# Optimization experiments

Hardware: AMD Instinct MI355X
Metric: run time of the kernel (lower is better)

The kernel has to match this reference:

```python
import jax, jax.numpy as jnp
import numpy as np

S, B, H, N, D = 1024, 4, 1024, 16, 64  # seq, batch, d_model, heads, head_dim
P = 2 * S  # relative position length (klen + qlen, no memory)


def rel_shift(x, klen):
    # x: [q, p, b, n] -> shift so position j aligns relatively, keep klen cols
    q, p, b, n = x.shape
    x = jnp.reshape(x, (p, q, b, n))[1:]
    x = jnp.reshape(x, (q, p - 1, b, n))[:, :klen]
    return x


def setup_inputs():
    key = jax.random.key(0)
    ks = jax.random.split(key, 12)
    f32 = jnp.float32
    attention_input = jax.random.normal(ks[0], (S, B, H), f32)
    pos_emb = jax.random.normal(ks[1], (P, B, H), f32)
    seg_embed = jax.random.normal(ks[2], (2, N, D), f32) * 0.02
    # segment matrix: one-hot of whether tokens i,j are in different segments
    seg_ids = jax.random.randint(ks[3], (S, B), 0, 2)
    diff = (seg_ids[:, None, :] != seg_ids[None, :, :]).astype(jnp.int32)
    seg_mat = jax.nn.one_hot(diff, 2, dtype=f32)  # [S,S,B,2]
    r_w_bias = jax.random.normal(ks[4], (N, D), f32) * 0.02
    r_r_bias = jax.random.normal(ks[5], (N, D), f32) * 0.02
    r_s_bias = jax.random.normal(ks[6], (N, D), f32) * 0.02
    # causal mask: 1 where attention is disallowed (j > i)
    causal = jnp.triu(jnp.ones((S, S), f32), k=1)
    attn_mask = jnp.broadcast_to(causal[:, :, None, None], (S, S, B, 1))
    w = lambda k: jax.random.normal(k, (H, N, D), f32) * 0.02
    return {
        'attention_input': attention_input, 'pos_emb': pos_emb,
        'seg_embed': seg_embed, 'seg_mat': seg_mat,
        'r_w_bias': r_w_bias, 'r_r_bias': r_r_bias, 'r_s_bias': r_s_bias,
        'attn_mask': attn_mask,
        'Wq': w(ks[7]), 'Wk': w(ks[8]), 'Wv': w(ks[9]),
        'Wr': w(ks[10]), 'Wo': w(ks[11]),
    }


def reference(attention_input, pos_emb, seg_embed, seg_mat, r_w_bias,
              r_r_bias, r_s_bias, attn_mask, Wq, Wk, Wv, Wr, Wo):
    scale = 1.0 / (D ** 0.5)
    q = jnp.einsum('ibh,hnd->ibnd', attention_input, Wq)
    k = jnp.einsum('ibh,hnd->ibnd', attention_input, Wk)
    v = jnp.einsum('ibh,hnd->ibnd', attention_input, Wv)
    kr = jnp.einsum('ibh,hnd->ibnd', pos_emb, Wr)  # [P,B,N,D]
    # content-based score
    ac = jnp.einsum('ibnd,jbnd->ijbn', q + r_w_bias, k)
    # position-based score with relative shift
    bd = jnp.einsum('ibnd,jbnd->ijbn', q + r_r_bias, kr)
    bd = rel_shift(bd, ac.shape[1])
    # segment-based score
    ef = jnp.einsum('ibnd,snd->ibns', q + r_s_bias, seg_embed)
    ef = jnp.einsum('ijbs,ibns->ijbn', seg_mat, ef)
    attn_score = (ac + bd + ef) * scale - 1e30 * attn_mask
    attn_prob = jax.nn.softmax(attn_score, axis=1)
    attn_vec = jnp.einsum('ijbn,jbnd->ibnd', attn_prob, v)
    attn_out = jnp.einsum('ibnd,hnd->ibh', attn_vec, Wo)
    return attn_out
```

## Files before the change

kernel.cpp:

```cpp
#include <hip/hip_runtime.h>
#include <hip/hip_bf16.h>
#include <stdint.h>


typedef short short8 __attribute__((ext_vector_type(8)));
typedef __bf16 bf16x8 __attribute__((ext_vector_type(8)));
typedef float f32x4 __attribute__((ext_vector_type(4)));
typedef unsigned short u16;
typedef unsigned long long u64;

#define LOG2E 1.4426950408889634f

__device__ __forceinline__ u16 f2bf(float f) {
  union { float f; unsigned u; } v; v.f = f;
  unsigned u = v.u;
  u += 0x7fffu + ((u >> 16) & 1u);
  return (u16)(u >> 16);
}
__device__ __forceinline__ float bf2f(u16 h) {
  union { unsigned u; float f; } v; v.u = ((unsigned)h) << 16;
  return v.f;
}

__device__ __forceinline__ f32x4 MFMA(short8 a, short8 b, f32x4 c) {
  union { short8 s; bf16x8 v; } ua, ub;
  ua.s = a; ub.s = b;
  return __builtin_amdgcn_mfma_f32_16x16x32_bf16(ua.v, ub.v, c, 0, 0, 0);
}

__device__ __forceinline__ void gload16(const void* g, void* l) {
  __builtin_amdgcn_global_load_lds(
      (const __attribute__((address_space(1))) unsigned int*)g,
      (__attribute__((address_space(3))) unsigned int*)l, 16, 0, 0);
}


__global__ void k_cvt3(const float* __restrict__ pos, const float* __restrict__ X,
                       const float* __restrict__ Wo, u16* __restrict__ Pb,
                       u16* __restrict__ Xb, u16* __restrict__ Wob) {
  int bid = blockIdx.x;
  const float* in; u16* out; int n, base;
  if (bid < 4101)      { in = pos; out = Pb;  n = 4198400; base = bid; }
  else if (bid < 8197) { in = X;   out = Xb;  n = 4194304; base = bid - 4101; }
  else                 { in = Wo;  out = Wob; n = 1048576; base = bid - 8197; }
  int i = (base * 256 + threadIdx.x) * 4;
  if (i >= n) return;
  float4 f = *reinterpret_cast<const float4*>(in + i);
  ushort4 o;
  o.x = f2bf(f.x); o.y = f2bf(f.y); o.z = f2bf(f.z); o.w = f2bf(f.w);
  *reinterpret_cast<ushort4*>(out + i) = o;
}

__global__ void k_transpose(const float* __restrict__ Wq, const float* __restrict__ Wk,
                            const float* __restrict__ Wv, const float* __restrict__ Wr,
                            u16* __restrict__ WT3, u16* __restrict__ WrT) {
  __shared__ float tile[32][33];
  int which = blockIdx.z;
  const float* src = (which == 0) ? Wq : (which == 1) ? Wk : (which == 2) ? Wv : Wr;
  u16* dst = (which < 3) ? (WT3 + (size_t)which * 1048576) : WrT;
  int c0 = blockIdx.x * 32, h0 = blockIdx.y * 32;
  int tx = threadIdx.x, ty = threadIdx.y;
  for (int r = 0; r < 32; r += 8)
    tile[ty + r][tx] = src[(size_t)(h0 + ty + r) * 1024 + c0 + tx];
  __syncthreads();
  for (int r = 0; r < 32; r += 8)
    dst[(size_t)(c0 + ty + r) * 1024 + h0 + tx] = f2bf(tile[tx][ty + r]);
}

__global__ void k_vt(const u16* __restrict__ V, u16* __restrict__ VT) {
  __shared__ u16 t[64][68];
  int i0 = blockIdx.x * 64;
  int bn = blockIdx.y;
  int tx = threadIdx.x;
  int ty = threadIdx.y;
#pragma unroll
  for (int q = 0; q < 16; q++) {
    int il = ty * 16 + q;
    t[il][tx] = V[(size_t)((bn << 10) + i0 + il) * 64 + tx];
  }
  __syncthreads();
#pragma unroll
  for (int q = 0; q < 16; q++) {
    int d = ty * 16 + q;
    VT[(((size_t)((bn << 6) | d)) << 10) + i0 + tx] = t[tx][d];
  }
}

__global__ void k_dpackw(const float* __restrict__ seg, u64* __restrict__ dpw) {
  int W = blockIdx.x * 4 + (threadIdx.x >> 6);
  int lane = threadIdx.x & 63;
  int jt = W & 15, i = W >> 4;
  const float4* p = reinterpret_cast<const float4*>(
      seg + ((size_t)((i << 10) + (jt << 6) + lane)) * 8);
  float4 a = p[0], bq = p[1];
  u64 m0 = __ballot(a.y != 0.f);
  u64 m1 = __ballot(a.w != 0.f);
  u64 m2 = __ballot(bq.y != 0.f);
  u64 m3 = __ballot(bq.w != 0.f);
  if (lane == 0) {
    int o = (i << 4) + jt;
    dpw[o] = m0;
    dpw[16384 + o] = m1;
    dpw[32768 + o] = m2;
    dpw[49152 + o] = m3;
  }
}

__global__ void k_ef(const u16* __restrict__ Q, const float* __restrict__ rsb,
                     const float* __restrict__ segE, float* __restrict__ ef) {
  int idx = blockIdx.x * blockDim.x + threadIdx.x;
  if (idx >= 65536) return;
  int n = (idx >> 10) & 15;
  float s0 = 0.f, s1 = 0.f;
  const short8* qrow = reinterpret_cast<const short8*>(Q + ((size_t)idx) * 64);
#pragma unroll
  for (int c = 0; c < 8; c++) {
    short8 v = qrow[c];
#pragma unroll
    for (int e = 0; e < 8; e++) {
      int d = c * 8 + e;
      float qv = bf2f((u16)v[e]) + rsb[n * 64 + d];
      s0 += qv * segE[n * 64 + d];
      s1 += qv * segE[1024 + n * 64 + d];
    }
  }
  ef[idx] = s0 * 0.125f;
  ef[65536 + idx] = s1 * 0.125f;
}


template <int MODE>
__device__ __forceinline__ int srcA(int row, int kk) {
  if (MODE == 0) return row * 1024 + kk;
  if (MODE == 1) return ((1024 - (row >> 2)) * 4 + (row & 3)) * 1024 + kk;
  int i = row >> 2, b = row & 3, n = kk >> 6, d = kk & 63;
  return (((b << 4) | n) * 1024 + i) * 64 + d;
}

template <int MODE>
__global__ __launch_bounds__(256, 2) void k_gemm(const u16* __restrict__ A,
                                                 const u16* __restrict__ L,
                                                 void* __restrict__ out0,
                                                 u16* __restrict__ outK,
                                                 u16* __restrict__ outV) {
  __shared__ u16 At[128 * 32];
  __shared__ u16 Lt[128 * 32];
  int m0 = blockIdx.x * 128, n0 = blockIdx.y * 128;
  int tid = threadIdx.x;
  int w = tid >> 6, lane = tid & 63;
  int lr = lane & 15, lg = lane >> 4;
  int wr = w >> 1, wc = w & 1;
  f32x4 acc[4][4] = {};

  for (int k0 = 0; k0 < 1024; k0 += 32) {
    for (int cc = 0; cc < 2; cc++) {
      int slot = cc * 256 + w * 64 + lane;
      int row = slot >> 2, ch = slot & 3;
      int sch = ch ^ ((row >> 1) & 3);
      gload16(A + srcA<MODE>(m0 + row, k0 + sch * 8), &At[(cc * 256 + w * 64) * 8]);
      gload16(L + (size_t)(n0 + row) * 1024 + k0 + sch * 8, &Lt[(cc * 256 + w * 64) * 8]);
    }
    __syncthreads();
    short8 af[4], bfr[4];
    for (int mt = 0; mt < 4; mt++) {
      int rr = wr * 64 + mt * 16 + lr;
      af[mt] = *reinterpret_cast<const short8*>(&At[rr * 32 + ((lg ^ ((rr >> 1) & 3)) * 8)]);
    }
    for (int ct = 0; ct < 4; ct++) {
      int rr = wc * 64 + ct * 16 + lr;
      bfr[ct] = *reinterpret_cast<const short8*>(&Lt[rr * 32 + ((lg ^ ((rr >> 1) & 3)) * 8)]);
    }
    for (int mt = 0; mt < 4; mt++)
      for (int ct = 0; ct < 4; ct++)
        acc[mt][ct] = MFMA(af[mt], bfr[ct], acc[mt][ct]);
    __syncthreads();
  }

  for (int mt = 0; mt < 4; mt++)
    for (int ct = 0; ct < 4; ct++)
      for (int r = 0; r < 4; r++) {
        int row = m0 + wr * 64 + mt * 16 + lg * 4 + r;
        int col = n0 + wc * 64 + ct * 16 + lr;
        float v = acc[mt][ct][r];
        if (MODE == 0) {
          int i = row >> 2, b = row & 3;
          int which = col >> 10, nd = col & 1023, n = nd >> 6, d = nd & 63;
          u16 hv = f2bf(v);
          int bn = (b << 4) | n;
          if (which == 0)       ((u16*)out0)[(size_t)(bn * 1024 + i) * 64 + d] = hv;
          else if (which == 1)  outK[(size_t)(bn * 1024 + i) * 64 + d] = hv;
          else                  outV[(size_t)(bn * 1024 + i) * 64 + d] = hv;
        } else if (MODE == 1) {
          int dist = row >> 2, b = row & 3, n = col >> 6, d = col & 63;
          ((u16*)out0)[(size_t)((((b << 4) | n) * 1024 + dist)) * 64 + d] = f2bf(v);
        } else {
          ((float*)out0)[(size_t)row * 1024 + col] = v;
        }
      }
}

__global__ __launch_bounds__(256, 2) void k_attn3(
    const u16* __restrict__ Q, const u16* __restrict__ K, const u16* __restrict__ VT,
    const u16* __restrict__ R, const float* __restrict__ ef,
    const u64* __restrict__ dpw, const float* __restrict__ rwb,
    const float* __restrict__ rrb, float* __restrict__ lsb, u16* __restrict__ pO) {
  __shared__ u16 sK[2][64][64];
  __shared__ u16 sV[2][64][64];
  __shared__ u16 sR[2][128][64];
  __shared__ u16 p_lds[4][16][64];
  int f = blockIdx.x + 40 * blockIdx.y;
  int wg = (f & 7) * 320 + (f >> 3);
  int bn = wg / 40;
  int cid = 39 - (wg - bn * 40);
  int b = bn >> 4, n = bn & 15;
  int g = (cid < 4) ? 0 : (cid < 12) ? 1 : (cid < 24) ? 2 : 3;
  int off = cid - 2 * g * (g + 1);
  int qt = 4 * g + off / (g + 1);
  int jc = off % (g + 1);
  int ntiles = (jc < g) ? 4 : (qt + 1 - 4 * g);
  int jt0 = jc * 4;
  int tid = threadIdx.x;
  int w = tid >> 6, lane = tid & 63;
  int lr = lane & 15, lg = lane >> 4;
  int qbase = qt * 64 + w * 16;
  int sub = lane >> 3, ch = lane & 7;
  int cs = (ch ^ sub) * 8;
  int r8 = lr & 7;

  auto stage = [&](int bi, int j0) {
    int rbase = qt * 64 - j0 - 63;
#pragma unroll
    for (int q = 0; q < 2; q++) {
      int row = w * 16 + q * 8 + sub;
      gload16(K + (size_t)((bn << 10) + j0 + row) * 64 + cs, &sK[bi][w * 16 + q * 8][0]);
      gload16(VT + (((size_t)((bn << 6) + row)) << 10) + j0 + cs, &sV[bi][w * 16 + q * 8][0]);
    }
#pragma unroll
    for (int q = 0; q < 4; q++) {
      int pr = w * 32 + q * 8 + sub;
      int ridx = rbase + pr;
      ridx = ridx < 0 ? 0 : (ridx > 1023 ? 1023 : ridx);
      gload16(R + (size_t)((bn << 10) + ridx) * 64 + cs, &sR[bi][w * 32 + q * 8][0]);
    }
  };

  stage(0, jt0 * 64);

  const u64* dwbase = dpw + ((size_t)((b << 10) + qbase + lg * 4) << 4);
  u64 dwc[4], dwn[4] = {0, 0, 0, 0};
#pragma unroll
  for (int r = 0; r < 4; r++) dwc[r] = dwbase[(r << 4) + jt0];

  short8 qw[2], qr[2];
  for (int ks = 0; ks < 2; ks++) {
    short8 qv = *reinterpret_cast<const short8*>(
        &Q[(size_t)((bn << 10) + qbase + lr) * 64 + ks * 32 + lg * 8]);
    short8 aa, bb;
    for (int e = 0; e < 8; e++) {
      int d = ks * 32 + lg * 8 + e;
      float fq = bf2f((u16)qv[e]);
      aa[e] = (short)f2bf((fq + rwb[n * 64 + d]) * 0.125f);
      bb[e] = (short)f2bf((fq + rrb[n * 64 + d]) * 0.125f);
    }
    qw[ks] = aa;
    qr[ks] = bb;
  }
  short8 ones;
#pragma unroll
  for (int e = 0; e < 8; e++) ones[e] = (short)0x3F80;
  float e0[4], de[4];
  for (int r = 0; r < 4; r++) {
    int qi = qbase + lg * 4 + r;
    e0[r] = ef[(bn << 10) + qi];
    de[r] = ef[65536 + (bn << 10) + qi] - e0[r];
  }
  float lsum[4] = {0.f, 0.f, 0.f, 0.f};
  f32x4 Oacc[4] = {};

  for (int t = 0; t < ntiles; t++) {
    int jt = jt0 + t;
    int j0 = jt * 64;
    int bi = t & 1;
    asm volatile("s_waitcnt vmcnt(0)" ::: "memory");
    __syncthreads();
    if (t + 1 < ntiles) {
      stage(bi ^ 1, j0 + 64);
#pragma unroll
      for (int r = 0; r < 4; r++) dwn[r] = dwbase[(r << 4) + jt + 1];
    }

    f32x4 sacc[4] = {};
    f32x4 tacc[5] = {};
    __builtin_amdgcn_s_setprio(1);
#pragma unroll
    for (int ks = 0; ks < 2; ks++) {
#pragma unroll
      for (int ct = 0; ct < 4; ct++) {
        short8 kb = *reinterpret_cast<const short8*>(
            &sK[bi][ct * 16 + lr][((ks * 4 + lg) ^ r8) * 8]);
        sacc[ct] = MFMA(qw[ks], kb, sacc[ct]);
      }
#pragma unroll
      for (int ct = 0; ct < 5; ct++) {
        short8 rb = *reinterpret_cast<const short8*>(
            &sR[bi][w * 16 + ct * 16 + lr][((ks * 4 + lg) ^ r8) * 8]);
        tacc[ct] = MFMA(qr[ks], rb, tacc[ct]);
      }
    }
    __builtin_amdgcn_s_setprio(0);

    bool diag = (jt == qt);
#pragma unroll
    for (int r = 0; r < 4; r++) {
      int ii = lg * 4 + r;
      int C0 = 63 + ii - lr;
      int sl = (lg << 4) | (C0 & 15);
      bool hi = (C0 >> 4) == 3;
      float tp0 = __shfl(tacc[0][r], sl);
      float tp1 = __shfl(tacc[1][r], sl);
      float tp2 = __shfl(tacc[2][r], sl);
      float tp3 = __shfl(tacc[3][r], sl);
      float tp4 = __shfl(tacc[4][r], sl);
#pragma unroll
      for (int ct = 0; ct < 4; ct++) {
        float bd;
        if (ct == 0)      bd = hi ? tp3 : tp4;
        else if (ct == 1) bd = hi ? tp2 : tp3;
        else if (ct == 2) bd = hi ? tp1 : tp2;
        else              bd = hi ? tp0 : tp1;
        float s = sacc[ct][r] + bd + e0[r];
        int jj = ct * 16 + lr;
        if ((dwc[r] >> jj) & 1) s += de[r];
        if (diag && jj > w * 16 + ii) s = -1.0e30f;
        sacc[ct][r] = exp2f(s * LOG2E);
      }
    }
#pragma unroll
    for (int ct = 0; ct < 4; ct++)
#pragma unroll
      for (int r = 0; r < 4; r++) {
        int ii = lg * 4 + r, jj = ct * 16 + lr;
        p_lds[w][ii][jj ^ ((ii & 7) << 3)] = f2bf(sacc[ct][r]);
      }
    f32x4 so = {};
    __builtin_amdgcn_s_setprio(1);
#pragma unroll
    for (int ks = 0; ks < 2; ks++) {
      int chunk = ks * 4 + lg;
      short8 afr = *reinterpret_cast<const short8*>(&p_lds[w][lr][(chunk ^ (lr & 7)) * 8]);
      so = MFMA(afr, ones, so);
#pragma unroll
      for (int dt = 0; dt < 4; dt++) {
        short8 vb = *reinterpret_cast<const short8*>(
            &sV[bi][dt * 16 + lr][((ks * 4 + lg) ^ r8) * 8]);
        Oacc[dt] = MFMA(afr, vb, Oacc[dt]);
      }
    }
    __builtin_amdgcn_s_setprio(0);
#pragma unroll
    for (int r = 0; r < 4; r++) lsum[r] += so[r];
#pragma unroll
    for (int r = 0; r < 4; r++) dwc[r] = dwn[r];
  }

  int pid = bn * 40 + cid;
  if (lr == 0)
#pragma unroll
    for (int r = 0; r < 4; r++) {
      int row = w * 16 + lg * 4 + r;
      lsb[(size_t)pid * 64 + row] = lsum[r];
    }
#pragma unroll
  for (int dt = 0; dt < 4; dt++)
#pragma unroll
    for (int r = 0; r < 4; r++) {
      int row = w * 16 + lg * 4 + r;
      pO[(size_t)pid * 4096 + row * 64 + dt * 16 + lr] = f2bf(Oacc[dt][r]);
    }
}

__global__ void k_comb(const float* __restrict__ lsb, const u16* __restrict__ pO,
                       u16* __restrict__ AV) {
  __shared__ float sinv[64];
  int qt = blockIdx.x, bn = blockIdx.y;
  int g = qt >> 2, nc = g + 1;
  int cbase = 2 * g * (g + 1) + (qt - 4 * g) * (g + 1);
  int pid0 = bn * 40 + cbase;
  int t = threadIdx.x;
  if (t < 64) {
    float L = 0.f;
    for (int c2 = 0; c2 < 4; c2++)
      if (c2 < nc) L += lsb[(size_t)(pid0 + c2) * 64 + t];
    sinv[t] = 1.0f / L;
  }
  __syncthreads();
  int dg = t & 7, rowg = t >> 3;
  for (int half = 0; half < 2; half++) {
    int ii = half * 32 + rowg;
    float o[8] = {0, 0, 0, 0, 0, 0, 0, 0};
    for (int c2 = 0; c2 < 4; c2++) {
      if (c2 >= nc) break;
      short8 pv = *reinterpret_cast<const short8*>(
          &pO[(size_t)(pid0 + c2) * 4096 + ii * 64 + dg * 8]);
      for (int e2 = 0; e2 < 8; e2++) o[e2] += bf2f((u16)pv[e2]);
    }
    float s = sinv[ii];
    short8 ov;
    for (int e2 = 0; e2 < 8; e2++) ov[e2] = (short)f2bf(o[e2] * s);
    *reinterpret_cast<short8*>(&AV[(size_t)((bn << 10) + qt * 64 + ii) * 64 + dg * 8]) = ov;
  }
}


extern "C" void kernel_launch(void* const* d_in, const int* in_sizes, int n_in,
                              void* d_out, int out_size, void* d_ws, size_t ws_size,
                              hipStream_t stream) {
  const float* X    = (const float*)d_in[0];
  const float* pos  = (const float*)d_in[1];
  const float* segE = (const float*)d_in[2];
  const float* segM = (const float*)d_in[3];
  const float* rwb  = (const float*)d_in[4];
  const float* rrb  = (const float*)d_in[5];
  const float* rsb  = (const float*)d_in[6];
  const float* Wq = (const float*)d_in[8];
  const float* Wk = (const float*)d_in[9];
  const float* Wv = (const float*)d_in[10];
  const float* Wr = (const float*)d_in[11];
  const float* Wo = (const float*)d_in[12];

  char* ws = (char*)d_ws;
  u16* Xb   = (u16*)(ws);
  u16* Pb   = (u16*)(ws + (8L << 20));
  u16* WT3  = (u16*)(ws + (24L << 20));
  u16* WrT  = (u16*)(ws + (30L << 20));
  u16* Wob  = (u16*)(ws + (32L << 20));
  u16* Qb   = (u16*)(ws + (34L << 20));
  u16* Kb   = (u16*)(ws + (42L << 20));
  u16* VTb  = (u16*)(ws + (50L << 20));
  u16* Rb   = (u16*)(ws + (58L << 20));
  float* efb = (float*)(ws + (66L << 20));
  u64* dpwb = (u64*)(ws + (66L << 20) + (512L << 10));
  float* lsbb = (float*)(ws + (67L << 20));
  u16* pOb  = (u16*)(ws + (69L << 20));
  u16* AVb  = Xb;
  u16* Vtmp = Pb;

  k_cvt3<<<9221, 256, 0, stream>>>(pos, X, Wo, Pb, Xb, Wob);
  k_transpose<<<dim3(32, 32, 4), dim3(32, 8), 0, stream>>>(Wq, Wk, Wv, Wr, WT3, WrT);
  k_gemm<1><<<dim3(32, 8), 256, 0, stream>>>(Pb, WrT, Rb, nullptr, nullptr);
  k_dpackw<<<4096, 256, 0, stream>>>(segM, dpwb);
  k_gemm<0><<<dim3(32, 24), 256, 0, stream>>>(Xb, WT3, Qb, Kb, Vtmp);
  k_vt<<<dim3(16, 64), dim3(64, 4), 0, stream>>>(Vtmp, VTb);
  k_ef<<<256, 256, 0, stream>>>(Qb, rsb, segE, efb);
  k_attn3<<<dim3(40, 64), 256, 0, stream>>>(Qb, Kb, VTb, Rb, efb, dpwb, rwb, rrb, lsbb, pOb);
  k_comb<<<dim3(16, 64), 256, 0, stream>>>(lsbb, pOb, AVb);
  k_gemm<2><<<dim3(32, 8), 256, 0, stream>>>(AVb, Wob, d_out, nullptr, nullptr);
}
```

Measured before the change: 177.9 us.

## Merge prep kernels, fuse QKV and R GEMMs, write single-chunk attention output directly

Merges the conversion, weight transpose and segment-bitmask kernels into one launch, and the V transpose plus ef kernels into another. Runs the QKV and positional-key GEMMs in one grid. Folds log2(e) into the Q scaling and ef so the exp2 needs no extra multiply. Attention blocks whose query tile has a single key chunk now normalize and write AV directly, so the combine kernel skips those tiles. This cuts launch count and tail idle time between small kernels, at the cost of branchy, heterogeneous blocks in the merged kernels.

```diff
diff --git a/kernel.cpp b/kernel.cpp
--- a/kernel.cpp
+++ b/kernel.cpp
@@ -34,118 +34,130 @@
       (__attribute__((address_space(3))) unsigned int*)l, 16, 0, 0);
 }
 
-
-__global__ void k_cvt3(const float* __restrict__ pos, const float* __restrict__ X,
-                       const float* __restrict__ Wo, u16* __restrict__ Pb,
-                       u16* __restrict__ Xb, u16* __restrict__ Wob) {
+__global__ void k_prep(const float* __restrict__ pos, const float* __restrict__ X,
+                       const float* __restrict__ Wo, const float* __restrict__ Wq,
+                       const float* __restrict__ Wk, const float* __restrict__ Wv,
+                       const float* __restrict__ Wr, const float* __restrict__ seg,
+                       u16* __restrict__ Pb, u16* __restrict__ Xb, u16* __restrict__ Wob,
+                       u16* __restrict__ WT3, u16* __restrict__ WrT, u64* __restrict__ dpw) {
   int bid = blockIdx.x;
-  const float* in; u16* out; int n, base;
-  if (bid < 4101)      { in = pos; out = Pb;  n = 4198400; base = bid; }
-  else if (bid < 8197) { in = X;   out = Xb;  n = 4194304; base = bid - 4101; }
-  else                 { in = Wo;  out = Wob; n = 1048576; base = bid - 8197; }
-  int i = (base * 256 + threadIdx.x) * 4;
-  if (i >= n) return;
-  float4 f = *reinterpret_cast<const float4*>(in + i);
-  ushort4 o;
-  o.x = f2bf(f.x); o.y = f2bf(f.y); o.z = f2bf(f.z); o.w = f2bf(f.w);
-  *reinterpret_cast<ushort4*>(out + i) = o;
-}
-
-__global__ void k_transpose(const float* __restrict__ Wq, const float* __restrict__ Wk,
-                            const float* __restrict__ Wv, const float* __restrict__ Wr,
-                            u16* __restrict__ WT3, u16* __restrict__ WrT) {
-  __shared__ float tile[32][33];
-  int which = blockIdx.z;
-  const float* src = (which == 0) ? Wq : (which == 1) ? Wk : (which == 2) ? Wv : Wr;
-  u16* dst = (which < 3) ? (WT3 + (size_t)which * 1048576) : WrT;
-  int c0 = blockIdx.x * 32, h0 = blockIdx.y * 32;
-  int tx = threadIdx.x, ty = threadIdx.y;
-  for (int r = 0; r < 32; r += 8)
-    tile[ty + r][tx] = src[(size_t)(h0 + ty + r) * 1024 + c0 + tx];
-  __syncthreads();
-  for (int r = 0; r < 32; r += 8)
-    dst[(size_t)(c0 + ty + r) * 1024 + h0 + tx] = f2bf(tile[tx][ty + r]);
-}
-
-__global__ void k_vt(const u16* __restrict__ V, u16* __restrict__ VT) {
-  __shared__ u16 t[64][68];
-  int i0 = blockIdx.x * 64;
-  int bn = blockIdx.y;
-  int tx = threadIdx.x;
-  int ty = threadIdx.y;
-#pragma unroll
-  for (int q = 0; q < 16; q++) {
-    int il = ty * 16 + q;
-    t[il][tx] = V[(size_t)((bn << 10) + i0 + il) * 64 + tx];
-  }
-  __syncthreads();
-#pragma unroll
-  for (int q = 0; q < 16; q++) {
-    int d = ty * 16 + q;
-    VT[(((size_t)((bn << 6) | d)) << 10) + i0 + tx] = t[tx][d];
-  }
-}
-
-__global__ void k_dpackw(const float* __restrict__ seg, u64* __restrict__ dpw) {
-  int W = blockIdx.x * 4 + (threadIdx.x >> 6);
-  int lane = threadIdx.x & 63;
-  int jt = W & 15, i = W >> 4;
-  const float4* p = reinterpret_cast<const float4*>(
-      seg + ((size_t)((i << 10) + (jt << 6) + lane)) * 8);
-  float4 a = p[0], bq = p[1];
-  u64 m0 = __ballot(a.y != 0.f);
-  u64 m1 = __ballot(a.w != 0.f);
-  u64 m2 = __ballot(bq.y != 0.f);
-  u64 m3 = __ballot(bq.w != 0.f);
-  if (lane == 0) {
-    int o = (i << 4) + jt;
-    dpw[o] = m0;
-    dpw[16384 + o] = m1;
-    dpw[32768 + o] = m2;
-    dpw[49152 + o] = m3;
-  }
-}
-
-__global__ void k_ef(const u16* __restrict__ Q, const float* __restrict__ rsb,
-                     const float* __restrict__ segE, float* __restrict__ ef) {
-  int idx = blockIdx.x * blockDim.x + threadIdx.x;
-  if (idx >= 65536) return;
-  int n = (idx >> 10) & 15;
-  float s0 = 0.f, s1 = 0.f;
-  const short8* qrow = reinterpret_cast<const short8*>(Q + ((size_t)idx) * 64);
-#pragma unroll
-  for (int c = 0; c < 8; c++) {
-    short8 v = qrow[c];
-#pragma unroll
-    for (int e = 0; e < 8; e++) {
-      int d = c * 8 + e;
-      float qv = bf2f((u16)v[e]) + rsb[n * 64 + d];
-      s0 += qv * segE[n * 64 + d];
-      s1 += qv * segE[1024 + n * 64 + d];
-    }
-  }
-  ef[idx] = s0 * 0.125f;
-  ef[65536 + idx] = s1 * 0.125f;
-}
-
-
-template <int MODE>
-__device__ __forceinline__ int srcA(int row, int kk) {
-  if (MODE == 0) return row * 1024 + kk;
-  if (MODE == 1) return ((1024 - (row >> 2)) * 4 + (row & 3)) * 1024 + kk;
+  int tid = threadIdx.x;
+  if (bid < 9221) {
+    const float* in; u16* out; int n, base;
+    if (bid < 4101)      { in = pos; out = Pb;  n = 4198400; base = bid; }
+    else if (bid < 8197) { in = X;   out = Xb;  n = 4194304; base = bid - 4101; }
+    else                 { in = Wo;  out = Wob; n = 1048576; base = bid - 8197; }
+    int i = (base * 256 + tid) * 4;
+    if (i >= n) return;
+    float4 f = *reinterpret_cast<const float4*>(in + i);
+    ushort4 o;
+    o.x = f2bf(f.x); o.y = f2bf(f.y); o.z = f2bf(f.z); o.w = f2bf(f.w);
+    *reinterpret_cast<ushort4*>(out + i) = o;
+  } else if (bid < 13317) {
+    __shared__ float tile[32][33];
+    int tb = bid - 9221;
+    int which = tb >> 10;
+    int by = (tb >> 5) & 31, bx = tb & 31;
+    const float* src = (which == 0) ? Wq : (which == 1) ? Wk : (which == 2) ? Wv : Wr;
+    u16* dst = (which < 3) ? (WT3 + (size_t)which * 1048576) : WrT;
+    int c0 = bx * 32, h0 = by * 32;
+    int tx = tid & 31, ty = tid >> 5;
+    for (int r = 0; r < 32; r += 8)
+      tile[ty + r][tx] = src[(size_t)(h0 + ty + r) * 1024 + c0 + tx];
+    __syncthreads();
+    for (int r = 0; r < 32; r += 8)
+      dst[(size_t)(c0 + ty + r) * 1024 + h0 + tx] = f2bf(tile[tx][ty + r]);
+  } else {
+    int W = (bid - 13317) * 4 + (tid >> 6);
+    int lane = tid & 63;
+    int jt = W & 15, i = W >> 4;
+    const float4* p = reinterpret_cast<const float4*>(
+        seg + ((size_t)((i << 10) + (jt << 6) + lane)) * 8);
+    float4 a = p[0], bq = p[1];
+    u64 m0 = __ballot(a.y != 0.f);
+    u64 m1 = __ballot(a.w != 0.f);
+    u64 m2 = __ballot(bq.y != 0.f);
+    u64 m3 = __ballot(bq.w != 0.f);
+    if (lane == 0) {
+      int o = (i << 4) + jt;
+      dpw[o] = m0;
+      dpw[16384 + o] = m1;
+      dpw[32768 + o] = m2;
+      dpw[49152 + o] = m3;
+    }
+  }
+}
+
+__global__ void k_mid(const u16* __restrict__ V, u16* __restrict__ VT,
+                      const u16* __restrict__ Q, const float* __restrict__ rsb,
+                      const float* __restrict__ segE, float* __restrict__ ef) {
+  int bid = blockIdx.x;
+  int tid = threadIdx.x;
+  if (bid < 1024) {
+    __shared__ u16 t[64][68];
+    int i0 = (bid & 15) * 64;
+    int bn = bid >> 4;
+    int tx = tid & 63, ty = tid >> 6;
+#pragma unroll
+    for (int q = 0; q < 16; q++) {
+      int il = ty * 16 + q;
+      t[il][tx] = V[(size_t)((bn << 10) + i0 + il) * 64 + tx];
+    }
+    __syncthreads();
+#pragma unroll
+    for (int q = 0; q < 16; q++) {
+      int d = ty * 16 + q;
+      VT[(((size_t)((bn << 6) | d)) << 10) + i0 + tx] = t[tx][d];
+    }
+  } else {
+    int idx = (bid - 1024) * 256 + tid;
+    int n = (idx >> 10) & 15;
+    float s0 = 0.f, s1 = 0.f;
+    const short8* qrow = reinterpret_cast<const short8*>(Q + ((size_t)idx) * 64);
+#pragma unroll
+    for (int c = 0; c < 8; c++) {
+      short8 v = qrow[c];
+#pragma unroll
+      for (int e = 0; e < 8; e++) {
+        int d = c * 8 + e;
+        float qv = bf2f((u16)v[e]) + rsb[n * 64 + d];
+        s0 += qv * segE[n * 64 + d];
+        s1 += qv * segE[1024 + n * 64 + d];
+      }
+    }
+    ef[idx] = s0 * (0.125f * LOG2E);
+    ef[65536 + idx] = s1 * (0.125f * LOG2E);
+  }
+}
+
+
+__device__ __forceinline__ int srcA_g(int mode, int row, int kk) {
+  if (mode == 0) return row * 1024 + kk;
+  if (mode == 1) return ((1024 - (row >> 2)) * 4 + (row & 3)) * 1024 + kk;
   int i = row >> 2, b = row & 3, n = kk >> 6, d = kk & 63;
   return (((b << 4) | n) * 1024 + i) * 64 + d;
 }
 
-template <int MODE>
-__global__ __launch_bounds__(256, 2) void k_gemm(const u16* __restrict__ A,
-                                                 const u16* __restrict__ L,
+template <int FUSED01>
+__global__ __launch_bounds__(256, 2) void k_gemm(const u16* __restrict__ A0,
+                                                 const u16* __restrict__ L0,
+                                                 const u16* __restrict__ A1,
+                                                 const u16* __restrict__ L1,
                                                  void* __restrict__ out0,
                                                  u16* __restrict__ outK,
-                                                 u16* __restrict__ outV) {
+                                                 u16* __restrict__ outV,
+                                                 u16* __restrict__ outR) {
   __shared__ u16 At[128 * 32];
   __shared__ u16 Lt[128 * 32];
-  int m0 = blockIdx.x * 128, n0 = blockIdx.y * 128;
+  int mode, n0;
+  const u16 *A, *L;
+  if (FUSED01) {
+    if (blockIdx.y < 24) { mode = 0; n0 = blockIdx.y * 128; A = A0; L = L0; }
+    else                 { mode = 1; n0 = (blockIdx.y - 24) * 128; A = A1; L = L1; }
+  } else {
+    mode = 2; n0 = blockIdx.y * 128; A = A0; L = L0;
+  }
+  int m0 = blockIdx.x * 128;
   int tid = threadIdx.x;
   int w = tid >> 6, lane = tid & 63;
   int lr = lane & 15, lg = lane >> 4;
@@ -157,7 +169,7 @@
       int slot = cc * 256 + w * 64 + lane;
       int row = slot >> 2, ch = slot & 3;
       int sch = ch ^ ((row >> 1) & 3);
-      gload16(A + srcA<MODE>(m0 + row, k0 + sch * 8), &At[(cc * 256 + w * 64) * 8]);
+      gload16(A + srcA_g(mode, m0 + row, k0 + sch * 8), &At[(cc * 256 + w * 64) * 8]);
       gload16(L + (size_t)(n0 + row) * 1024 + k0 + sch * 8, &Lt[(cc * 256 + w * 64) * 8]);
     }
     __syncthreads();
@@ -182,7 +194,7 @@
         int row = m0 + wr * 64 + mt * 16 + lg * 4 + r;
         int col = n0 + wc * 64 + ct * 16 + lr;
         float v = acc[mt][ct][r];
-        if (MODE == 0) {
+        if (FUSED01 && mode == 0) {
           int i = row >> 2, b = row & 3;
           int which = col >> 10, nd = col & 1023, n = nd >> 6, d = nd & 63;
           u16 hv = f2bf(v);
@@ -190,9 +202,9 @@
           if (which == 0)       ((u16*)out0)[(size_t)(bn * 1024 + i) * 64 + d] = hv;
           else if (which == 1)  outK[(size_t)(bn * 1024 + i) * 64 + d] = hv;
           else                  outV[(size_t)(bn * 1024 + i) * 64 + d] = hv;
-        } else if (MODE == 1) {
+        } else if (FUSED01) {
           int dist = row >> 2, b = row & 3, n = col >> 6, d = col & 63;
-          ((u16*)out0)[(size_t)((((b << 4) | n) * 1024 + dist)) * 64 + d] = f2bf(v);
+          outR[(size_t)((((b << 4) | n) * 1024 + dist)) * 64 + d] = f2bf(v);
         } else {
           ((float*)out0)[(size_t)row * 1024 + col] = v;
         }
@@ -203,7 +215,8 @@
     const u16* __restrict__ Q, const u16* __restrict__ K, const u16* __restrict__ VT,
     const u16* __restrict__ R, const float* __restrict__ ef,
     const u64* __restrict__ dpw, const float* __restrict__ rwb,
-    const float* __restrict__ rrb, float* __restrict__ lsb, u16* __restrict__ pO) {
+    const float* __restrict__ rrb, float* __restrict__ lsb, u16* __restrict__ pO,
+    u16* __restrict__ AV) {
   __shared__ u16 sK[2][64][64];
   __shared__ u16 sV[2][64][64];
   __shared__ u16 sR[2][128][64];
@@ -251,6 +264,7 @@
 #pragma unroll
   for (int r = 0; r < 4; r++) dwc[r] = dwbase[(r << 4) + jt0];
 
+  const float QS = 0.125f * LOG2E;
   short8 qw[2], qr[2];
   for (int ks = 0; ks < 2; ks++) {
     short8 qv = *reinterpret_cast<const short8*>(
@@ -259,8 +273,8 @@
     for (int e = 0; e < 8; e++) {
       int d = ks * 32 + lg * 8 + e;
       float fq = bf2f((u16)qv[e]);
-      aa[e] = (short)f2bf((fq + rwb[n * 64 + d]) * 0.125f);
-      bb[e] = (short)f2bf((fq + rrb[n * 64 + d]) * 0.125f);
+      aa[e] = (short)f2bf((fq + rwb[n * 64 + d]) * QS);
+      bb[e] = (short)f2bf((fq + rrb[n * 64 + d]) * QS);
     }
     qw[ks] = aa;
     qr[ks] = bb;
@@ -332,7 +346,7 @@
         int jj = ct * 16 + lr;
         if ((dwc[r] >> jj) & 1) s += de[r];
         if (diag && jj > w * 16 + ii) s = -1.0e30f;
-        sacc[ct][r] = exp2f(s * LOG2E);
+        sacc[ct][r] = exp2f(s);
       }
     }
 #pragma unroll
@@ -363,26 +377,39 @@
     for (int r = 0; r < 4; r++) dwc[r] = dwn[r];
   }
 
-  int pid = bn * 40 + cid;
-  if (lr == 0)
-#pragma unroll
-    for (int r = 0; r < 4; r++) {
-      int row = w * 16 + lg * 4 + r;
-      lsb[(size_t)pid * 64 + row] = lsum[r];
-    }
-#pragma unroll
-  for (int dt = 0; dt < 4; dt++)
-#pragma unroll
-    for (int r = 0; r < 4; r++) {
-      int row = w * 16 + lg * 4 + r;
-      pO[(size_t)pid * 4096 + row * 64 + dt * 16 + lr] = f2bf(Oacc[dt][r]);
-    }
+  if (g == 0) {
+    float inv[4];
+#pragma unroll
+    for (int r = 0; r < 4; r++) inv[r] = 1.0f / lsum[r];
+#pragma unroll
+    for (int dt = 0; dt < 4; dt++)
+#pragma unroll
+      for (int r = 0; r < 4; r++) {
+        int qi = qbase + lg * 4 + r;
+        AV[(size_t)((bn << 10) + qi) * 64 + dt * 16 + lr] = f2bf(Oacc[dt][r] * inv[r]);
+      }
+  } else {
+    int pid = bn * 40 + cid;
+    if (lr == 0)
+#pragma unroll
+      for (int r = 0; r < 4; r++) {
+        int row = w * 16 + lg * 4 + r;
+        lsb[(size_t)pid * 64 + row] = lsum[r];
+      }
+#pragma unroll
+    for (int dt = 0; dt < 4; dt++)
+#pragma unroll
+      for (int r = 0; r < 4; r++) {
+        int row = w * 16 + lg * 4 + r;
+        pO[(size_t)pid * 4096 + row * 64 + dt * 16 + lr] = f2bf(Oacc[dt][r]);
+      }
+  }
 }
 
 __global__ void k_comb(const float* __restrict__ lsb, const u16* __restrict__ pO,
                        u16* __restrict__ AV) {
   __shared__ float sinv[64];
-  int qt = blockIdx.x, bn = blockIdx.y;
+  int qt = blockIdx.x + 4, bn = blockIdx.y;
   int g = qt >> 2, nc = g + 1;
   int cbase = 2 * g * (g + 1) + (qt - 4 * g) * (g + 1);
   int pid0 = bn * 40 + cbase;
@@ -443,16 +470,15 @@
   float* lsbb = (float*)(ws + (67L << 20));
   u16* pOb  = (u16*)(ws + (69L << 20));
   u16* AVb  = Xb;
-  u16* Vtmp = Pb;
-
-  k_cvt3<<<9221, 256, 0, stream>>>(pos, X, Wo, Pb, Xb, Wob);
-  k_transpose<<<dim3(32, 32, 4), dim3(32, 8), 0, stream>>>(Wq, Wk, Wv, Wr, WT3, WrT);
-  k_gemm<1><<<dim3(32, 8), 256, 0, stream>>>(Pb, WrT, Rb, nullptr, nullptr);
-  k_dpackw<<<4096, 256, 0, stream>>>(segM, dpwb);
-  k_gemm<0><<<dim3(32, 24), 256, 0, stream>>>(Xb, WT3, Qb, Kb, Vtmp);
-  k_vt<<<dim3(16, 64), dim3(64, 4), 0, stream>>>(Vtmp, VTb);
-  k_ef<<<256, 256, 0, stream>>>(Qb, rsb, segE, efb);
-  k_attn3<<<dim3(40, 64), 256, 0, stream>>>(Qb, Kb, VTb, Rb, efb, dpwb, rwb, rrb, lsbb, pOb);
-  k_comb<<<dim3(16, 64), 256, 0, stream>>>(lsbb, pOb, AVb);
-  k_gemm<2><<<dim3(32, 8), 256, 0, stream>>>(AVb, Wob, d_out, nullptr, nullptr);
-}
+  u16* Vtmp = pOb;
+
+  k_prep<<<17413, 256, 0, stream>>>(pos, X, Wo, Wq, Wk, Wv, Wr, segM,
+                                    Pb, Xb, Wob, WT3, WrT, dpwb);
+  k_gemm<1><<<dim3(32, 32), 256, 0, stream>>>(Xb, WT3, Pb, WrT, Qb, Kb, Vtmp, Rb);
+  k_mid<<<1280, 256, 0, stream>>>(Vtmp, VTb, Qb, rsb, segE, efb);
+  k_attn3<<<dim3(40, 64), 256, 0, stream>>>(Qb, Kb, VTb, Rb, efb, dpwb, rwb, rrb,
+                                            lsbb, pOb, AVb);
+  k_comb<<<dim3(12, 64), 256, 0, stream>>>(lsbb, pOb, AVb);
+  k_gemm<0><<<dim3(32, 8), 256, 0, stream>>>(AVb, Wob, nullptr, nullptr,
+                                             d_out, nullptr, nullptr, nullptr);
+}
```

Result: faster. 164.3 us (-7.7%).
